# Kernel optimization log

Measured on AMD Instinct MI355X. Metric: run time of the kernel, lower is better.

Reference implementation:

```python
import jax, jax.numpy as jnp
import numpy as np

TIER_BITS = [16, 8, 6, 4]


def quantize_ste(x, bits):
    # Fake-quant with straight-through estimator; per-tensor abs-max scale.
    if bits >= 16:
        return x
    max_val = float(2 ** (bits - 1) - 1)
    scale = jnp.maximum(jnp.max(jnp.abs(x)), 1e-8) / max_val
    x_q = jnp.clip(jnp.round(x / scale), -max_val, max_val) * scale
    return x + jax.lax.stop_gradient(x_q - x)


def setup_inputs() -> dict:
    key = jax.random.key(0)
    ks = jax.random.split(key, 6)
    dim = 1024
    sizes = [256, 2048 - 256, 16384 - 2048, 50257 - 16384]  # tier row counts
    tws = [jax.random.normal(ks[i], (sizes[i], dim), dtype=jnp.float32) * 0.02 for i in range(4)]
    input_ids = jax.random.randint(ks[4], (8, 2048), 0, 50257, dtype=jnp.int64)
    return {
        "input_ids": input_ids,
        "tw0": tws[0], "tw1": tws[1], "tw2": tws[2], "tw3": tws[3],
        "ts0": jnp.ones((1, dim), jnp.float32) * 0.1,
        "ts1": jnp.ones((1, dim), jnp.float32) * 0.1,
        "ts2": jnp.ones((1, dim), jnp.float32) * 0.1,
        "ts3": jnp.ones((1, dim), jnp.float32) * 0.1,
    }


def reference(input_ids, tw0, tw1, tw2, tw3, ts0, ts1, ts2, ts3):
    tws = [tw0, tw1, tw2, tw3]
    tss = [ts0, ts1, ts2, ts3]
    # Rebuild the full fake-quantized vocab table (same math as the torch module),
    # then gather the requested rows.
    table = jnp.concatenate(
        [quantize_ste(tws[i] * tss[i], TIER_BITS[i]) for i in range(4)], axis=0
    )  # [vocab, dim]
    return jnp.take(table, input_ids, axis=0)  # [B, S, dim]
```

## Files before the change

kernel.cpp:

```cpp
#include <hip/hip_runtime.h>

#define DIM 1024
#define D4  (DIM / 4)

typedef float vfloat4 __attribute__((ext_vector_type(4)));

static __device__ __forceinline__ vfloat4 nt_load4(const vfloat4* p) {
    return __builtin_nontemporal_load(p);
}
static __device__ __forceinline__ vfloat4 abs_max4(vfloat4 m, vfloat4 v) {
    m.x = fmaxf(m.x, fabsf(v.x)); m.y = fmaxf(m.y, fabsf(v.y));
    m.z = fmaxf(m.z, fabsf(v.z)); m.w = fmaxf(m.w, fabsf(v.w));
    return m;
}

__global__ __launch_bounds__(256) void absmax3_kernel(
    const vfloat4* __restrict__ tw1, const vfloat4* __restrict__ ts1, long n1,
    const vfloat4* __restrict__ tw2, const vfloat4* __restrict__ ts2, long n2,
    const vfloat4* __restrict__ tw3, const vfloat4* __restrict__ ts3, long n3,
    int b1, int b2, unsigned* __restrict__ amax)
{
    __shared__ float smax[4];
    int bid = blockIdx.x;
    const vfloat4 *tw, *ts; long n4; int blo, bhi; unsigned* out;
    if (bid < b1)      { tw = tw1; ts = ts1; n4 = n1; blo = 0;  bhi = b1;        out = amax + 0; }
    else if (bid < b2) { tw = tw2; ts = ts2; n4 = n2; blo = b1; bhi = b2;        out = amax + 1; }
    else               { tw = tw3; ts = ts3; n4 = n3; blo = b2; bhi = gridDim.x; out = amax + 2; }

    int  nb    = bhi - blo;
    long chunk = (n4 + nb - 1) / nb;
    long start = (long)(bid - blo) * chunk;
    long end   = start + chunk; if (end > n4) end = n4;
    int  t     = threadIdx.x;

    vfloat4 m0 = {0,0,0,0}, m1 = {0,0,0,0}, m2 = {0,0,0,0}, m3 = {0,0,0,0};
    vfloat4 m4 = {0,0,0,0}, m5 = {0,0,0,0}, m6 = {0,0,0,0}, m7 = {0,0,0,0};

    long base = start;
    for (; base + 2048 <= end; base += 2048) {
        vfloat4 p0 = nt_load4(tw + base +    0 + t);
        vfloat4 p1 = nt_load4(tw + base +  256 + t);
        vfloat4 p2 = nt_load4(tw + base +  512 + t);
        vfloat4 p3 = nt_load4(tw + base +  768 + t);
        vfloat4 p4 = nt_load4(tw + base + 1024 + t);
        vfloat4 p5 = nt_load4(tw + base + 1280 + t);
        vfloat4 p6 = nt_load4(tw + base + 1536 + t);
        vfloat4 p7 = nt_load4(tw + base + 1792 + t);
        m0 = abs_max4(m0, p0); m1 = abs_max4(m1, p1);
        m2 = abs_max4(m2, p2); m3 = abs_max4(m3, p3);
        m4 = abs_max4(m4, p4); m5 = abs_max4(m5, p5);
        m6 = abs_max4(m6, p6); m7 = abs_max4(m7, p7);
    }
    for (long i = base + t; i < end; i += 256)
        m0 = abs_max4(m0, nt_load4(tw + i));

    m0 = abs_max4(m0, m1); m2 = abs_max4(m2, m3);
    m4 = abs_max4(m4, m5); m6 = abs_max4(m6, m7);
    m0 = abs_max4(m0, m2); m4 = abs_max4(m4, m6);
    m0 = abs_max4(m0, m4);

    vfloat4 s = ts[(start + t) & (D4 - 1)];
    float m = fmaxf(fmaxf(m0.x * fabsf(s.x), m0.y * fabsf(s.y)),
                    fmaxf(m0.z * fabsf(s.z), m0.w * fabsf(s.w)));

    for (int off = 32; off > 0; off >>= 1)
        m = fmaxf(m, __shfl_down(m, off));
    if ((threadIdx.x & 63) == 0) smax[threadIdx.x >> 6] = m;
    __syncthreads();
    if (threadIdx.x == 0) {
        float bm = fmaxf(fmaxf(smax[0], smax[1]), fmaxf(smax[2], smax[3]));
        atomicMax(out, __float_as_uint(bm));
    }
}

__global__ __launch_bounds__(256) void gather_quant_kernel(
    const int* __restrict__ ids, int n_tokens,
    const float* __restrict__ tw0, const float* __restrict__ tw1,
    const float* __restrict__ tw2, const float* __restrict__ tw3,
    const float* __restrict__ ts0, const float* __restrict__ ts1,
    const float* __restrict__ ts2, const float* __restrict__ ts3,
    const unsigned* __restrict__ amax, float* __restrict__ out)
{
    int sub  = threadIdx.x >> 6;
    int lane = threadIdx.x & 63;
    int token = blockIdx.x * 4 + sub;
    if (token >= n_tokens) return;
    int id = ids[token];

    const float* tw; const float* ts;
    float maxval = 1.f; unsigned am = 0; bool quant = true;
    if (id < 256)        { tw = tw0 + (long)id * DIM;           ts = ts0; quant = false; }
    else if (id < 2048)  { tw = tw1 + (long)(id - 256) * DIM;   ts = ts1; maxval = 127.f; am = amax[0]; }
    else if (id < 16384) { tw = tw2 + (long)(id - 2048) * DIM;  ts = ts2; maxval = 31.f;  am = amax[1]; }
    else                 { tw = tw3 + (long)(id - 16384) * DIM; ts = ts3; maxval = 7.f;   am = amax[2]; }

    const vfloat4* twv = (const vfloat4*)tw;
    const vfloat4* tsv = (const vfloat4*)ts;

    vfloat4 v0 = nt_load4(twv + lane +   0), v1 = nt_load4(twv + lane +  64);
    vfloat4 v2 = nt_load4(twv + lane + 128), v3 = nt_load4(twv + lane + 192);
    vfloat4 s0 = tsv[lane +   0], s1 = tsv[lane +  64];
    vfloat4 s2 = tsv[lane + 128], s3 = tsv[lane + 192];

    float scale = fmaxf(__uint_as_float(am), 1e-8f) / maxval;

    vfloat4 vv[4] = {v0, v1, v2, v3};
    vfloat4 ss[4] = {s0, s1, s2, s3};
    float* outp = out + (long)token * DIM;
    #pragma unroll
    for (int j = 0; j < 4; ++j) {
        vfloat4 x = vv[j] * ss[j];
        if (quant) {
            x.x = fminf(fmaxf(rintf(x.x / scale), -maxval), maxval) * scale;
            x.y = fminf(fmaxf(rintf(x.y / scale), -maxval), maxval) * scale;
            x.z = fminf(fmaxf(rintf(x.z / scale), -maxval), maxval) * scale;
            x.w = fminf(fmaxf(rintf(x.w / scale), -maxval), maxval) * scale;
        }
        __builtin_nontemporal_store(x, (vfloat4*)outp + lane + 64 * j);
    }
}

extern "C" void kernel_launch(void* const* d_in, const int* in_sizes, int n_in,
                              void* d_out, int out_size, void* d_ws, size_t ws_size,
                              hipStream_t stream) {
    const int*   ids = (const int*)d_in[0];
    const float* tw0 = (const float*)d_in[1];
    const float* tw1 = (const float*)d_in[2];
    const float* tw2 = (const float*)d_in[3];
    const float* tw3 = (const float*)d_in[4];
    const float* ts0 = (const float*)d_in[5];
    const float* ts1 = (const float*)d_in[6];
    const float* ts2 = (const float*)d_in[7];
    const float* ts3 = (const float*)d_in[8];
    float* out = (float*)d_out;

    unsigned* amax = (unsigned*)d_ws;
    (void)hipMemsetAsync(d_ws, 0, 3 * sizeof(unsigned), stream);

    long n1 = (long)in_sizes[2] / 4;
    long n2 = (long)in_sizes[3] / 4;
    long n3 = (long)in_sizes[4] / 4;
    long N  = n1 + n2 + n3;

    const int G = 2048;
    int b1 = (int)((n1 * G + N - 1) / N); if (b1 < 1) b1 = 1;
    int b2 = b1 + (int)((n2 * G) / N);    if (b2 <= b1) b2 = b1 + 1;
    if (b2 >= G) b2 = G - 1;

    absmax3_kernel<<<G, 256, 0, stream>>>(
        (const vfloat4*)tw1, (const vfloat4*)ts1, n1,
        (const vfloat4*)tw2, (const vfloat4*)ts2, n2,
        (const vfloat4*)tw3, (const vfloat4*)ts3, n3,
        b1, b2, amax);

    int n_tokens = in_sizes[0];
    gather_quant_kernel<<<(n_tokens + 3) / 4, 256, 0, stream>>>(
        ids, n_tokens, tw0, tw1, tw2, tw3, ts0, ts1, ts2, ts3, amax, out);
}
```

Before: 283.1 us.

## Replace memset and atomics with per-block slots; gather two tokens per wave

```diff
diff --git a/kernel.cpp b/kernel.cpp
--- a/kernel.cpp
+++ b/kernel.cpp
@@ -13,19 +13,26 @@
     m.z = fmaxf(m.z, fabsf(v.z)); m.w = fmaxf(m.w, fabsf(v.w));
     return m;
 }
+static __device__ __forceinline__ vfloat4 fq4(vfloat4 x, float sc, float mv) {
+    x.x = fminf(fmaxf(rintf(x.x / sc), -mv), mv) * sc;
+    x.y = fminf(fmaxf(rintf(x.y / sc), -mv), mv) * sc;
+    x.z = fminf(fmaxf(rintf(x.z / sc), -mv), mv) * sc;
+    x.w = fminf(fmaxf(rintf(x.w / sc), -mv), mv) * sc;
+    return x;
+}
 
 __global__ __launch_bounds__(256) void absmax3_kernel(
     const vfloat4* __restrict__ tw1, const vfloat4* __restrict__ ts1, long n1,
     const vfloat4* __restrict__ tw2, const vfloat4* __restrict__ ts2, long n2,
     const vfloat4* __restrict__ tw3, const vfloat4* __restrict__ ts3, long n3,
-    int b1, int b2, unsigned* __restrict__ amax)
+    int b1, int b2, float* __restrict__ ws, int slots)
 {
     __shared__ float smax[4];
     int bid = blockIdx.x;
-    const vfloat4 *tw, *ts; long n4; int blo, bhi; unsigned* out;
-    if (bid < b1)      { tw = tw1; ts = ts1; n4 = n1; blo = 0;  bhi = b1;        out = amax + 0; }
-    else if (bid < b2) { tw = tw2; ts = ts2; n4 = n2; blo = b1; bhi = b2;        out = amax + 1; }
-    else               { tw = tw3; ts = ts3; n4 = n3; blo = b2; bhi = gridDim.x; out = amax + 2; }
+    const vfloat4 *tw, *ts; long n4; int blo, bhi, tier;
+    if (bid < b1)      { tw = tw1; ts = ts1; n4 = n1; blo = 0;  bhi = b1;        tier = 0; }
+    else if (bid < b2) { tw = tw2; ts = ts2; n4 = n2; blo = b1; bhi = b2;        tier = 1; }
+    else               { tw = tw3; ts = ts3; n4 = n3; blo = b2; bhi = gridDim.x; tier = 2; }
 
     int  nb    = bhi - blo;
     long chunk = (n4 + nb - 1) / nb;
@@ -69,7 +76,8 @@
     __syncthreads();
     if (threadIdx.x == 0) {
         float bm = fmaxf(fmaxf(smax[0], smax[1]), fmaxf(smax[2], smax[3]));
-        atomicMax(out, __float_as_uint(bm));
+        if (slots) ws[bid] = bm;
+        else       atomicMax((unsigned*)ws + tier, __float_as_uint(bm));
     }
 }
 
@@ -79,44 +87,90 @@
     const float* __restrict__ tw2, const float* __restrict__ tw3,
     const float* __restrict__ ts0, const float* __restrict__ ts1,
     const float* __restrict__ ts2, const float* __restrict__ ts3,
-    const unsigned* __restrict__ amax, float* __restrict__ out)
+    const float* __restrict__ ws, int nslots, int b1, int b2,
+    float* __restrict__ out)
 {
-    int sub  = threadIdx.x >> 6;
+    __shared__ float amax_s[3];
+    __shared__ float wred[4][3];
+    int wid  = threadIdx.x >> 6;
     int lane = threadIdx.x & 63;
-    int token = blockIdx.x * 4 + sub;
-    if (token >= n_tokens) return;
-    int id = ids[token];
-
-    const float* tw; const float* ts;
-    float maxval = 1.f; unsigned am = 0; bool quant = true;
-    if (id < 256)        { tw = tw0 + (long)id * DIM;           ts = ts0; quant = false; }
-    else if (id < 2048)  { tw = tw1 + (long)(id - 256) * DIM;   ts = ts1; maxval = 127.f; am = amax[0]; }
-    else if (id < 16384) { tw = tw2 + (long)(id - 2048) * DIM;  ts = ts2; maxval = 31.f;  am = amax[1]; }
-    else                 { tw = tw3 + (long)(id - 16384) * DIM; ts = ts3; maxval = 7.f;   am = amax[2]; }
-
-    const vfloat4* twv = (const vfloat4*)tw;
-    const vfloat4* tsv = (const vfloat4*)ts;
-
-    vfloat4 v0 = nt_load4(twv + lane +   0), v1 = nt_load4(twv + lane +  64);
-    vfloat4 v2 = nt_load4(twv + lane + 128), v3 = nt_load4(twv + lane + 192);
-    vfloat4 s0 = tsv[lane +   0], s1 = tsv[lane +  64];
-    vfloat4 s2 = tsv[lane + 128], s3 = tsv[lane + 192];
-
-    float scale = fmaxf(__uint_as_float(am), 1e-8f) / maxval;
-
-    vfloat4 vv[4] = {v0, v1, v2, v3};
-    vfloat4 ss[4] = {s0, s1, s2, s3};
-    float* outp = out + (long)token * DIM;
-    #pragma unroll
-    for (int j = 0; j < 4; ++j) {
-        vfloat4 x = vv[j] * ss[j];
-        if (quant) {
-            x.x = fminf(fmaxf(rintf(x.x / scale), -maxval), maxval) * scale;
-            x.y = fminf(fmaxf(rintf(x.y / scale), -maxval), maxval) * scale;
-            x.z = fminf(fmaxf(rintf(x.z / scale), -maxval), maxval) * scale;
-            x.w = fminf(fmaxf(rintf(x.w / scale), -maxval), maxval) * scale;
+
+    if (nslots > 0) {
+        float r0 = 0.f, r1 = 0.f, r2 = 0.f;
+        for (int s = threadIdx.x; s < nslots; s += 256) {
+            float v = ws[s];
+            if      (s < b1) r0 = fmaxf(r0, v);
+            else if (s < b2) r1 = fmaxf(r1, v);
+            else             r2 = fmaxf(r2, v);
         }
-        __builtin_nontemporal_store(x, (vfloat4*)outp + lane + 64 * j);
+        #pragma unroll
+        for (int off = 32; off > 0; off >>= 1) {
+            r0 = fmaxf(r0, __shfl_down(r0, off));
+            r1 = fmaxf(r1, __shfl_down(r1, off));
+            r2 = fmaxf(r2, __shfl_down(r2, off));
+        }
+        if (lane == 0) { wred[wid][0] = r0; wred[wid][1] = r1; wred[wid][2] = r2; }
+        __syncthreads();
+        if (threadIdx.x < 3)
+            amax_s[threadIdx.x] = fmaxf(fmaxf(wred[0][threadIdx.x], wred[1][threadIdx.x]),
+                                        fmaxf(wred[2][threadIdx.x], wred[3][threadIdx.x]));
+    } else {
+        if (threadIdx.x < 3) amax_s[threadIdx.x] = ws[threadIdx.x];
+    }
+    __syncthreads();
+
+    int tA = blockIdx.x * 8 + wid * 2;
+    int tB = tA + 1;
+    bool okA = tA < n_tokens, okB = tB < n_tokens;
+    int idA = okA ? ids[tA] : 0;
+    int idB = okB ? ids[tB] : 0;
+
+    const float *pA, *pB; const vfloat4 *tsA, *tsB;
+    float mvA = 1.f, mvB = 1.f, amA = 1.f, amB = 1.f; bool qA = true, qB = true;
+
+    if (idA < 256)        { pA = tw0 + (long)idA * DIM;           tsA = (const vfloat4*)ts0; qA = false; }
+    else if (idA < 2048)  { pA = tw1 + (long)(idA - 256) * DIM;   tsA = (const vfloat4*)ts1; mvA = 127.f; amA = amax_s[0]; }
+    else if (idA < 16384) { pA = tw2 + (long)(idA - 2048) * DIM;  tsA = (const vfloat4*)ts2; mvA = 31.f;  amA = amax_s[1]; }
+    else                  { pA = tw3 + (long)(idA - 16384) * DIM; tsA = (const vfloat4*)ts3; mvA = 7.f;   amA = amax_s[2]; }
+
+    if (idB < 256)        { pB = tw0 + (long)idB * DIM;           tsB = (const vfloat4*)ts0; qB = false; }
+    else if (idB < 2048)  { pB = tw1 + (long)(idB - 256) * DIM;   tsB = (const vfloat4*)ts1; mvB = 127.f; amB = amax_s[0]; }
+    else if (idB < 16384) { pB = tw2 + (long)(idB - 2048) * DIM;  tsB = (const vfloat4*)ts2; mvB = 31.f;  amB = amax_s[1]; }
+    else                  { pB = tw3 + (long)(idB - 16384) * DIM; tsB = (const vfloat4*)ts3; mvB = 7.f;   amB = amax_s[2]; }
+
+    const vfloat4* wvA = (const vfloat4*)pA + lane;
+    const vfloat4* wvB = (const vfloat4*)pB + lane;
+    vfloat4 a0 = nt_load4(wvA +   0), a1 = nt_load4(wvA +  64);
+    vfloat4 a2 = nt_load4(wvA + 128), a3 = nt_load4(wvA + 192);
+    vfloat4 c0 = nt_load4(wvB +   0), c1 = nt_load4(wvB +  64);
+    vfloat4 c2 = nt_load4(wvB + 128), c3 = nt_load4(wvB + 192);
+    vfloat4 sA0 = tsA[lane +   0], sA1 = tsA[lane +  64];
+    vfloat4 sA2 = tsA[lane + 128], sA3 = tsA[lane + 192];
+    vfloat4 sB0 = tsB[lane +   0], sB1 = tsB[lane +  64];
+    vfloat4 sB2 = tsB[lane + 128], sB3 = tsB[lane + 192];
+
+    float scA = fmaxf(amA, 1e-8f) / mvA;
+    float scB = fmaxf(amB, 1e-8f) / mvB;
+
+    if (okA) {
+        vfloat4* op = (vfloat4*)(out + (long)tA * DIM) + lane;
+        vfloat4 x0 = a0 * sA0, x1 = a1 * sA1, x2 = a2 * sA2, x3 = a3 * sA3;
+        if (qA) { x0 = fq4(x0, scA, mvA); x1 = fq4(x1, scA, mvA);
+                  x2 = fq4(x2, scA, mvA); x3 = fq4(x3, scA, mvA); }
+        __builtin_nontemporal_store(x0, op +   0);
+        __builtin_nontemporal_store(x1, op +  64);
+        __builtin_nontemporal_store(x2, op + 128);
+        __builtin_nontemporal_store(x3, op + 192);
+    }
+    if (okB) {
+        vfloat4* op = (vfloat4*)(out + (long)tB * DIM) + lane;
+        vfloat4 x0 = c0 * sB0, x1 = c1 * sB1, x2 = c2 * sB2, x3 = c3 * sB3;
+        if (qB) { x0 = fq4(x0, scB, mvB); x1 = fq4(x1, scB, mvB);
+                  x2 = fq4(x2, scB, mvB); x3 = fq4(x3, scB, mvB); }
+        __builtin_nontemporal_store(x0, op +   0);
+        __builtin_nontemporal_store(x1, op +  64);
+        __builtin_nontemporal_store(x2, op + 128);
+        __builtin_nontemporal_store(x3, op + 192);
     }
 }
 
@@ -134,9 +188,6 @@
     const float* ts3 = (const float*)d_in[8];
     float* out = (float*)d_out;
 
-    unsigned* amax = (unsigned*)d_ws;
-    (void)hipMemsetAsync(d_ws, 0, 3 * sizeof(unsigned), stream);
-
     long n1 = (long)in_sizes[2] / 4;
     long n2 = (long)in_sizes[3] / 4;
     long n3 = (long)in_sizes[4] / 4;
@@ -147,13 +198,18 @@
     int b2 = b1 + (int)((n2 * G) / N);    if (b2 <= b1) b2 = b1 + 1;
     if (b2 >= G) b2 = G - 1;
 
+    int use_slots = (ws_size >= (size_t)G * sizeof(float)) ? 1 : 0;
+    if (!use_slots)
+        (void)hipMemsetAsync(d_ws, 0, 3 * sizeof(unsigned), stream);
+
     absmax3_kernel<<<G, 256, 0, stream>>>(
         (const vfloat4*)tw1, (const vfloat4*)ts1, n1,
         (const vfloat4*)tw2, (const vfloat4*)ts2, n2,
         (const vfloat4*)tw3, (const vfloat4*)ts3, n3,
-        b1, b2, amax);
+        b1, b2, (float*)d_ws, use_slots);
 
     int n_tokens = in_sizes[0];
-    gather_quant_kernel<<<(n_tokens + 3) / 4, 256, 0, stream>>>(
-        ids, n_tokens, tw0, tw1, tw2, tw3, ts0, ts1, ts2, ts3, amax, out);
-}
+    gather_quant_kernel<<<(n_tokens + 7) / 8, 256, 0, stream>>>(
+        ids, n_tokens, tw0, tw1, tw2, tw3, ts0, ts1, ts2, ts3,
+        (const float*)d_ws, use_slots ? G : 0, b1, b2, out);
+}
```

Result: faster. 276.4 us (-2.4%).
